# Performance work log

Hardware: AMD Instinct MI355X
Metric: run time of the kernel (lower is better)

## Reference

```python
import jax, jax.numpy as jnp
from jax import lax
import numpy as np

B, W, M, F = 8, 20, 512, 16
H = 128          # n_hidden
HALF = 64        # half_hid
K = 10           # conv out channels
LONG_K = W // 2  # dilated conv kernel


def setup_inputs() -> dict:
    key = jax.random.key(0)
    ks = jax.random.split(key, 24)
    s = 0.1  # weight scale (xavier-ish)
    return {
        "X": jax.random.normal(ks[0], (B, W, M, F), jnp.float32),
        "Y": jax.random.uniform(ks[1], (B, M), jnp.float32),
        "adj": jax.random.uniform(ks[2], (M, M), jnp.float32),
        "V": jax.random.normal(ks[3], (HALF,), jnp.float32) * s,
        "bv": jax.random.normal(ks[4], (1,), jnp.float32) * s,
        "W1": jax.random.normal(ks[5], (HALF, H), jnp.float32) * s,
        "b1": jax.random.normal(ks[6], (HALF,), jnp.float32) * s,
        "W2": jax.random.normal(ks[7], (HALF, H), jnp.float32) * s,
        "Wb": jax.random.normal(ks[8], (M, M), jnp.float32) * s,
        "wb": jax.random.normal(ks[9], (1,), jnp.float32) * s,
        "conv_w": jax.random.normal(ks[10], (K, F, W), jnp.float32) * s,
        "conv_b": jax.random.normal(ks[11], (K,), jnp.float32) * s,
        "convl_w": jax.random.normal(ks[12], (K, F, LONG_K), jnp.float32) * s,
        "convl_b": jax.random.normal(ks[13], (K,), jnp.float32) * s,
        "gru_Wih": jax.random.normal(ks[14], (3 * H, F), jnp.float32) * s,
        "gru_Whh": jax.random.normal(ks[15], (3 * H, H), jnp.float32) * s,
        "gru_bih": jax.random.normal(ks[16], (3 * H,), jnp.float32) * s,
        "gru_bhh": jax.random.normal(ks[17], (3 * H,), jnp.float32) * s,
        "gc1_W": jax.random.normal(ks[18], (3 * K, H), jnp.float32) * s,
        "gc1_b": jax.random.normal(ks[19], (H,), jnp.float32) * s,
        "gc2_W": jax.random.normal(ks[20], (H, K), jnp.float32) * s,
        "gc2_b": jax.random.normal(ks[21], (K,), jnp.float32) * s,
        "out_W": jax.random.normal(ks[22], (1, H + K), jnp.float32) * s,
        "out_b": jax.random.normal(ks[23], (1,), jnp.float32) * s,
    }


def _gru_last(xseq, Wih, Whh, bih, bhh):
    # xseq: (N, T, F) -> last hidden (N, H), PyTorch GRU gate order r,z,n
    n_hid = Whh.shape[1]
    def step(h, x_t):
        gx = x_t @ Wih.T + bih
        gh = h @ Whh.T + bhh
        xr, xz, xn = jnp.split(gx, 3, axis=-1)
        hr, hz, hn = jnp.split(gh, 3, axis=-1)
        r = jax.nn.sigmoid(xr + hr)
        z = jax.nn.sigmoid(xz + hz)
        n = jnp.tanh(xn + r * hn)
        return (1.0 - z) * n + z * h, None
    h0 = jnp.zeros((xseq.shape[0], n_hid), xseq.dtype)
    hT, _ = lax.scan(step, h0, jnp.moveaxis(xseq, 1, 0))
    return hT


def _forward(X, Y, adj, V, bv, W1, b1, W2, Wb, wb, conv_w, conv_b, convl_w,
             convl_b, gru_Wih, gru_Whh, gru_bih, gru_bhh, gc1_W, gc1_b,
             gc2_W, gc2_b, out_W, out_b):
    b, w, m, f = X.shape
    # ---- temporal branch: GRU per node ----
    x = jnp.transpose(X, (0, 2, 1, 3)).reshape(b * m, w, f)
    last_hid = _gru_last(x, gru_Wih, gru_Whh, gru_bih, gru_bhh).reshape(b, m, -1)
    out_temporal = last_hid
    # ---- attention-style adaptive adjacency ----
    # hid_rpt_m[b,i,j]=last_hid[b,j]; hid_rpt_w[b,i,j]=last_hid[b,i]
    p1 = jnp.einsum('bjh,kh->bjk', last_hid, W1)  # pairs with column index j
    p2 = jnp.einsum('bih,kh->bik', last_hid, W2)  # pairs with row index i
    pre = p1[:, None, :, :] + p2[:, :, None, :] + b1  # (b,m,m,half)
    a_mx = jnp.einsum('bijk,k->bij', jax.nn.elu(pre), V) + bv[0]
    # F.normalize(p=2, dim=1)
    nrm = jnp.sqrt(jnp.sum(a_mx * a_mx, axis=1, keepdims=True))
    a_mx = a_mx / jnp.maximum(nrm, 1e-12)
    # ---- per-node conv1d (vectorized over nodes) ----
    Xc = jnp.transpose(X, (0, 2, 3, 1)).reshape(b * m, f, w)  # (bm, f, w)
    dn = ('NCH', 'OIH', 'NCH')
    r = lax.conv_general_dilated(Xc, conv_w, (1,), 'VALID', dimension_numbers=dn)
    r = r + conv_b[None, :, None]                      # (bm, K, 1)
    rl = lax.conv_general_dilated(Xc, convl_w, (1,), 'VALID',
                                  rhs_dilation=(2,), dimension_numbers=dn)
    rl = rl + convl_b[None, :, None]                   # (bm, K, long_out)
    r_cat = jnp.concatenate([r, rl], axis=-1)          # (bm, K, 1+long_out)
    r_l = jax.nn.relu(r_cat.reshape(b, m, -1))         # (b, m, (1+long_out)*K)
    # ---- gate learned adjacency with fixed adjacency ----
    c = jax.nn.sigmoid(jnp.einsum('bij,jk->bik', a_mx, Wb) + wb[0])
    A = adj[None] * c + a_mx * (1.0 - c)               # (b,m,m)
    # ---- graph convolutions: out = A @ (x @ W) + b ----
    h1 = jax.nn.relu(jnp.einsum('bij,bjh->bih', A, r_l @ gc1_W) + gc1_b)
    out_spatial = jax.nn.relu(jnp.einsum('bij,bjh->bih', A, h1 @ gc2_W) + gc2_b)
    # ---- readout ----
    out = jnp.concatenate([out_spatial, out_temporal], axis=-1)
    out = (out @ out_W.T + out_b).squeeze(-1)          # (b, m)
    y = out.reshape(-1)
    Yf = Y.reshape(-1)
    # BCE with logits: softplus(y) - Y*y, averaged
    loss = jnp.mean(jax.nn.softplus(y) - Yf * y)
    return loss, jax.nn.sigmoid(y)


def reference(X, Y, adj, V, bv, W1, b1, W2, Wb, wb, conv_w, conv_b, convl_w,
              convl_b, gru_Wih, gru_Whh, gru_bih, gru_bhh, gc1_W, gc1_b,
              gc2_W, gc2_b, out_W, out_b):
    return _forward(X, Y, adj, V, bv, W1, b1, W2, Wb, wb, conv_w, conv_b,
                    convl_w, convl_b, gru_Wih, gru_Whh, gru_bih, gru_bhh,
                    gc1_W, gc1_b, gc2_W, gc2_b, out_W, out_b)
```

## Files before the change

kernel.cpp:

```cpp
#include <hip/hip_runtime.h>
#include <math.h>

#define Bn 8
#define Wn 20
#define Mn 512
#define Fn 16
#define Hn 128
#define HALFn 64
#define Kn 10

typedef __attribute__((ext_vector_type(8))) short short8;
typedef __attribute__((ext_vector_type(4))) float f32x4;
typedef unsigned short ushort_t;

__device__ __forceinline__ float sigmoidf_(float x) {
  return 1.0f / (1.0f + __expf(-x));
}
__device__ __forceinline__ float tanhf_(float x) {
  float xx = fminf(fmaxf(x, -15.f), 15.f);
  float e = __expf(2.f * xx);
  return (e - 1.f) / (e + 1.f);
}
__device__ __forceinline__ float reluf_(float x) { return fmaxf(x, 0.f); }
__device__ __forceinline__ float eluf_(float x) {
  return (x > 0.f) ? x : (__expf(x) - 1.f);
}
__device__ __forceinline__ ushort_t bf16_rne(float v) {
  unsigned u = __float_as_uint(v);
  u += 0x7FFFu + ((u >> 16) & 1u);
  return (ushort_t)(u >> 16);
}
__device__ __forceinline__ float bf16_to_f(ushort_t b) {
  return __uint_as_float(((unsigned)b) << 16);
}

__global__ __launch_bounds__(256) void pack_kernel(
    const float* __restrict__ Whh, const float* __restrict__ Wih,
    const float* __restrict__ Wb, ushort_t* __restrict__ Bpack,
    ushort_t* __restrict__ WbT_hi, ushort_t* __restrict__ WbT_lo,
    float* __restrict__ ssq, float* __restrict__ d_out) {
  int tid = threadIdx.x;
  if (blockIdx.x < 240) {
    int idx = blockIdx.x * 256 + tid;
    if (idx < 4096) ssq[idx] = 0.f;
    if (idx == 0) d_out[0] = 0.f;
    if (idx >= 24 * 5 * 512) return;
    int j = idx & 7;
    int lane = (idx >> 3) & 63;
    int ks = (idx >> 9) % 5;
    int nt = idx / (5 * 512);
    int k = ks * 32 + (lane >> 4) * 8 + j;
    int g = (nt & 7) * 16 + (nt >> 3) * 128 + (lane & 15);
    float val = 0.f;
    if (k < 128) val = Whh[g * 128 + k];
    else if (k < 144) val = Wih[g * 16 + (k - 128)];
    ushort_t hb = bf16_rne(val);
    float lo = val - bf16_to_f(hb);
    Bpack[(((long)nt * 5 + ks) * 2 + 0) * 512 + lane * 8 + j] = hb;
    Bpack[(((long)nt * 5 + ks) * 2 + 1) * 512 + lane * 8 + j] = bf16_rne(lo);
  } else {
    int t = blockIdx.x - 240;
    int k0 = (t >> 3) * 64, j0 = (t & 7) * 64;
    __shared__ float wt[64][65];
    for (int idx = tid; idx < 4096; idx += 256) {
      int r = idx >> 6, c = idx & 63;
      wt[r][c] = Wb[(long)(k0 + r) * 512 + j0 + c];
    }
    __syncthreads();
    for (int idx = tid; idx < 4096; idx += 256) {
      int r = idx >> 6, c = idx & 63;
      float v = wt[c][r];
      ushort_t hb = bf16_rne(v);
      WbT_hi[(long)(j0 + r) * 512 + k0 + c] = hb;
      WbT_lo[(long)(j0 + r) * 512 + k0 + c] = bf16_rne(v - bf16_to_f(hb));
    }
  }
}

#define LDK 168
#define HSZ (16 * LDK)
__global__ __launch_bounds__(512, 2) void gru_kernel(
    const float* __restrict__ X, const ushort_t* __restrict__ Bpack,
    const float* __restrict__ bih, const float* __restrict__ bhh,
    const float* __restrict__ W1, const float* __restrict__ W2,
    const float* __restrict__ b1, float* __restrict__ last_hid,
    float* __restrict__ p1, float* __restrict__ p2) {
  const int tid = threadIdx.x;
  const int wave = tid >> 6;
  const int lane = tid & 63;
  const int quad = lane >> 4;
  const int jl = lane & 15;
  const int j0 = wave * 16;
  const int blk = blockIdx.x;
  const int b = blk >> 5;
  const int m0 = (blk & 31) * 16;

  __shared__ __align__(16) ushort_t smem_hs[4 * HSZ];

  short8 frR[5][2], frZ[5][2], frN[4][2], frXN[2];
#pragma unroll
  for (int ks = 0; ks < 5; ++ks) {
#pragma unroll
    for (int p = 0; p < 2; ++p) {
      frR[ks][p] = *(const short8*)&Bpack[(((long)(wave) * 5 + ks) * 2 + p) * 512 + lane * 8];
      frZ[ks][p] = *(const short8*)&Bpack[(((long)(8 + wave) * 5 + ks) * 2 + p) * 512 + lane * 8];
    }
  }
#pragma unroll
  for (int ks = 0; ks < 4; ++ks) {
#pragma unroll
    for (int p = 0; p < 2; ++p)
      frN[ks][p] = *(const short8*)&Bpack[(((long)(16 + wave) * 5 + ks) * 2 + p) * 512 + lane * 8];
  }
#pragma unroll
  for (int p = 0; p < 2; ++p)
    frXN[p] = *(const short8*)&Bpack[(((long)(16 + wave) * 5 + 4) * 2 + p) * 512 + lane * 8];

  const float cr  = bih[j0 + jl] + bhh[j0 + jl];
  const float cz  = bih[128 + j0 + jl] + bhh[128 + j0 + jl];
  const float cnx = bih[256 + j0 + jl];
  const float cnh = bhh[256 + j0 + jl];

  for (int i = tid; i < 4 * HSZ; i += 512) smem_hs[i] = 0;

  const float* Xb = X + (long)b * (Wn * Mn * Fn) + (long)m0 * Fn;
  float x0 = 0.f;
  if (tid < 256) x0 = Xb[tid];
  __syncthreads();
  if (tid < 256) {
    int s = tid >> 4, f = tid & 15;
    ushort_t hb = bf16_rne(x0);
    smem_hs[0 * HSZ + s * LDK + 128 + f] = hb;
    smem_hs[2 * HSZ + s * LDK + 128 + f] = bf16_rne(x0 - bf16_to_f(hb));
  }
  __syncthreads();

  float hp[4] = {0.f, 0.f, 0.f, 0.f};

  for (int t = 0; t < Wn; ++t) {
    const int cur = t & 1, nxt = cur ^ 1;
    const int hiC = cur * HSZ, loC = (2 + cur) * HSZ;
    const int hiN = nxt * HSZ, loN = (2 + nxt) * HSZ;
    float xpre = 0.f;
    if (tid < 256 && t < Wn - 1) xpre = Xb[(long)(t + 1) * (Mn * Fn) + tid];

    f32x4 aR[2], aZ[2], aHN[2], aXN;
    aR[0] = aR[1] = aZ[0] = aZ[1] = aHN[0] = aHN[1] = aXN = (f32x4){0.f, 0.f, 0.f, 0.f};
#pragma unroll
    for (int ks = 0; ks < 5; ++ks) {
      const int p = ks & 1;
      short8 ah = *(const short8*)&smem_hs[hiC + jl * LDK + ks * 32 + quad * 8];
      short8 al = *(const short8*)&smem_hs[loC + jl * LDK + ks * 32 + quad * 8];
      aR[p] = __builtin_amdgcn_mfma_f32_16x16x32_bf16(ah, frR[ks][0], aR[p], 0, 0, 0);
      aR[p] = __builtin_amdgcn_mfma_f32_16x16x32_bf16(ah, frR[ks][1], aR[p], 0, 0, 0);
      aR[p] = __builtin_amdgcn_mfma_f32_16x16x32_bf16(al, frR[ks][0], aR[p], 0, 0, 0);
      aZ[p] = __builtin_amdgcn_mfma_f32_16x16x32_bf16(ah, frZ[ks][0], aZ[p], 0, 0, 0);
      aZ[p] = __builtin_amdgcn_mfma_f32_16x16x32_bf16(ah, frZ[ks][1], aZ[p], 0, 0, 0);
      aZ[p] = __builtin_amdgcn_mfma_f32_16x16x32_bf16(al, frZ[ks][0], aZ[p], 0, 0, 0);
      if (ks < 4) {
        aHN[p] = __builtin_amdgcn_mfma_f32_16x16x32_bf16(ah, frN[ks][0], aHN[p], 0, 0, 0);
        aHN[p] = __builtin_amdgcn_mfma_f32_16x16x32_bf16(ah, frN[ks][1], aHN[p], 0, 0, 0);
        aHN[p] = __builtin_amdgcn_mfma_f32_16x16x32_bf16(al, frN[ks][0], aHN[p], 0, 0, 0);
      } else {
        aXN = __builtin_amdgcn_mfma_f32_16x16x32_bf16(ah, frXN[0], aXN, 0, 0, 0);
        aXN = __builtin_amdgcn_mfma_f32_16x16x32_bf16(ah, frXN[1], aXN, 0, 0, 0);
        aXN = __builtin_amdgcn_mfma_f32_16x16x32_bf16(al, frXN[0], aXN, 0, 0, 0);
      }
    }

#pragma unroll
    for (int reg = 0; reg < 4; ++reg) {
      float r = sigmoidf_(aR[0][reg] + aR[1][reg] + cr);
      float z = sigmoidf_(aZ[0][reg] + aZ[1][reg] + cz);
      float n = tanhf_(aXN[reg] + cnx + r * (aHN[0][reg] + aHN[1][reg] + cnh));
      float h = (1.f - z) * n + z * hp[reg];
      hp[reg] = h;
      int s = quad * 4 + reg;
      ushort_t hb = bf16_rne(h);
      smem_hs[hiN + s * LDK + j0 + jl] = hb;
      smem_hs[loN + s * LDK + j0 + jl] = bf16_rne(h - bf16_to_f(hb));
    }
    if (tid < 256 && t < Wn - 1) {
      int s = tid >> 4, f = tid & 15;
      ushort_t hb = bf16_rne(xpre);
      smem_hs[hiN + s * LDK + 128 + f] = hb;
      smem_hs[loN + s * LDK + 128 + f] = bf16_rne(xpre - bf16_to_f(hb));
    }
    __syncthreads();
  }

  float* hs_f = (float*)smem_hs;
#pragma unroll
  for (int reg = 0; reg < 4; ++reg) {
    int s = quad * 4 + reg;
    float h = hp[reg];
    last_hid[(long)(blk * 16 + s) * Hn + j0 + jl] = h;
    hs_f[s * 132 + j0 + jl] = h;
  }
  __syncthreads();
  {
    int k = tid & 63;
    int part = (tid >> 6) & 1;
    int sg = tid >> 7;
    const float* Wp = part ? W2 : W1;
    float a[4];
    float init = part ? 0.f : b1[k];
    a[0] = a[1] = a[2] = a[3] = init;
    for (int h = 0; h < 128; h += 4) {
      float4 w = *(const float4*)&Wp[k * 128 + h];
#pragma unroll
      for (int rr = 0; rr < 4; ++rr) {
        float4 q = *(const float4*)&hs_f[(sg * 4 + rr) * 132 + h];
        a[rr] += q.x * w.x + q.y * w.y + q.z * w.z + q.w * w.w;
      }
    }
    float* outp = part ? p2 : p1;
#pragma unroll
    for (int rr = 0; rr < 4; ++rr)
      outp[(long)(blk * 16 + sg * 4 + rr) * 64 + k] = a[rr];
  }
}

__global__ __launch_bounds__(128) void conv_t1_kernel(
    const float* __restrict__ X, const float* __restrict__ conv_w,
    const float* __restrict__ conv_b, const float* __restrict__ convl_w,
    const float* __restrict__ convl_b, const float* __restrict__ gc1_W,
    ushort_t* __restrict__ t1T_hi, ushort_t* __restrict__ t1T_lo) {
  int tid = threadIdx.x;
  int n0 = blockIdx.x * 8;
  int b = n0 >> 9, m0 = n0 & 511;
  __shared__ float xs[8][16][20];
  __shared__ float cw[3200];
  __shared__ float clw[1600];
  __shared__ float rs[8][32];
  for (int idx = tid; idx < 3200; idx += 128) cw[idx] = conv_w[idx];
  for (int idx = tid; idx < 1600; idx += 128) clw[idx] = convl_w[idx];
  for (int w = 0; w < 20; ++w)
    xs[tid >> 4][tid & 15][w] = X[((long)(b * 20 + w) * 512 + m0) * 16 + tid];
  __syncthreads();
  if (tid < 80) {
    int s = tid / 10, k = tid % 10;
    float a0 = conv_b[k];
    float l0 = convl_b[k], l1 = convl_b[k];
    for (int f = 0; f < 16; ++f) {
#pragma unroll
      for (int w = 0; w < 20; ++w) a0 = fmaf(xs[s][f][w], cw[k * 320 + f * 20 + w], a0);
#pragma unroll
      for (int q = 0; q < 10; ++q) {
        float wv = clw[k * 160 + f * 10 + q];
        l0 = fmaf(xs[s][f][2 * q], wv, l0);
        l1 = fmaf(xs[s][f][2 * q + 1], wv, l1);
      }
    }
    rs[s][k * 3 + 0] = reluf_(a0);
    rs[s][k * 3 + 1] = reluf_(l0);
    rs[s][k * 3 + 2] = reluf_(l1);
  }
  __syncthreads();
  float w[30];
#pragma unroll
  for (int q = 0; q < 30; ++q) w[q] = gc1_W[q * 128 + tid];
  long base = ((long)b * 128 + tid) * 512 + m0;
#pragma unroll
  for (int s = 0; s < 8; ++s) {
    float a = 0.f;
#pragma unroll
    for (int q = 0; q < 30; ++q) a = fmaf(rs[s][q], w[q], a);
    ushort_t hb = bf16_rne(a);
    t1T_hi[base + s] = hb;
    t1T_lo[base + s] = bf16_rne(a - bf16_to_f(hb));
  }
}

__global__ __launch_bounds__(256) void amx_kernel(
    const float* __restrict__ p1, const float* __restrict__ p2,
    const float* __restrict__ V, const float* __restrict__ bv,
    float* __restrict__ amx, float* __restrict__ ssq) {
  int tid = threadIdx.x;
  int j0 = blockIdx.x * 32, i0 = blockIdx.y * 32, bz = blockIdx.z;
  __shared__ float p1s[32][68];
  __shared__ float p2s[32][68];
  __shared__ float Vs[64];
  __shared__ float cred[16][33];
  if (tid < 64) Vs[tid] = V[tid];
  {
    int rr = tid >> 3, c0 = (tid & 7) * 8;
    *(float4*)&p1s[rr][c0]     = *(const float4*)&p1[(long)(bz * 512 + j0 + rr) * 64 + c0];
    *(float4*)&p1s[rr][c0 + 4] = *(const float4*)&p1[(long)(bz * 512 + j0 + rr) * 64 + c0 + 4];
    *(float4*)&p2s[rr][c0]     = *(const float4*)&p2[(long)(bz * 512 + i0 + rr) * 64 + c0];
    *(float4*)&p2s[rr][c0 + 4] = *(const float4*)&p2[(long)(bz * 512 + i0 + rr) * 64 + c0 + 4];
  }
  __syncthreads();
  int r0 = tid >> 4, c0 = tid & 15;
  float acc[2][2] = {{0.f, 0.f}, {0.f, 0.f}};
  for (int k = 0; k < 64; ++k) {
    float vj0 = p1s[c0][k], vj1 = p1s[c0 + 16][k];
    float vi0 = p2s[r0][k], vi1 = p2s[r0 + 16][k];
    float vk = Vs[k];
    acc[0][0] = fmaf(eluf_(vj0 + vi0), vk, acc[0][0]);
    acc[0][1] = fmaf(eluf_(vj1 + vi0), vk, acc[0][1]);
    acc[1][0] = fmaf(eluf_(vj0 + vi1), vk, acc[1][0]);
    acc[1][1] = fmaf(eluf_(vj1 + vi1), vk, acc[1][1]);
  }
  float bvv = bv[0];
  float s2[2] = {0.f, 0.f};
#pragma unroll
  for (int a = 0; a < 2; ++a)
#pragma unroll
    for (int c = 0; c < 2; ++c) {
      float v = acc[a][c] + bvv;
      amx[((long)(bz * 512 + i0 + r0 + a * 16)) * 512 + j0 + c0 + c * 16] = v;
      s2[c] += v * v;
    }
  cred[r0][c0] = s2[0];
  cred[r0][c0 + 16] = s2[1];
  __syncthreads();
  if (tid < 32) {
    float s = 0.f;
#pragma unroll
    for (int p = 0; p < 16; ++p) s += cred[p][tid];
    atomicAdd(&ssq[bz * 512 + j0 + tid], s);
  }
}

#define CPK 40
__global__ __launch_bounds__(128, 2) void gemm_cA(
    const float* __restrict__ amx, const ushort_t* __restrict__ WbT_hi,
    const ushort_t* __restrict__ WbT_lo, const float* __restrict__ adj,
    const float* __restrict__ wb, const float* __restrict__ ssq,
    float* __restrict__ A) {
  const int bz = blockIdx.z;
  const int i0 = blockIdx.y * 128;
  const int j0 = blockIdx.x * 64;
  const int tid = threadIdx.x;
  const int wave = tid >> 6;
  const int lane = tid & 63;
  const int quad = lane >> 4, jl = lane & 15;

  __shared__ __align__(16) ushort_t Ahi[128][CPK];
  __shared__ __align__(16) ushort_t Alo[128][CPK];
  __shared__ __align__(16) ushort_t Bhi[64][CPK];
  __shared__ __align__(16) ushort_t Blo[64][CPK];
  __shared__ float rs_s[512];

  const float* Abase = amx + (long)bz * 262144;
  const float* sb = ssq + bz * 512;
  for (int i = tid; i < 512; i += 128)
    rs_s[i] = 1.f / fmaxf(sqrtf(sb[i]), 1e-12f);

  f32x4 acc[4][4];
#pragma unroll
  for (int a = 0; a < 4; ++a)
#pragma unroll
    for (int c = 0; c < 4; ++c) acc[a][c] = (f32x4){0.f, 0.f, 0.f, 0.f};

  for (int kk0 = 0; kk0 < 512; kk0 += 32) {
    __syncthreads();
#pragma unroll
    for (int l = 0; l < 8; ++l) {
      int e = l * 512 + tid * 4;
      int r = e >> 5, kq = e & 31;
      float4 v = *(const float4*)&Abase[(long)(i0 + r) * 512 + kk0 + kq];
      float4 sc = *(const float4*)&rs_s[kk0 + kq];
      float vv[4] = {v.x * sc.x, v.y * sc.y, v.z * sc.z, v.w * sc.w};
#pragma unroll
      for (int q = 0; q < 4; ++q) {
        ushort_t hb = bf16_rne(vv[q]);
        Ahi[r][kq + q] = hb;
        Alo[r][kq + q] = bf16_rne(vv[q] - bf16_to_f(hb));
      }
    }
#pragma unroll
    for (int l = 0; l < 2; ++l) {
      int e = l * 1024 + tid * 8;
      int r = e >> 5, kc = e & 31;
      *(uint4*)&Bhi[r][kc] = *(const uint4*)&WbT_hi[(long)(j0 + r) * 512 + kk0 + kc];
      *(uint4*)&Blo[r][kc] = *(const uint4*)&WbT_lo[(long)(j0 + r) * 512 + kk0 + kc];
    }
    __syncthreads();
    short8 ah[4], al[4], bh[4], bl[4];
#pragma unroll
    for (int tm = 0; tm < 4; ++tm) {
      ah[tm] = *(const short8*)&Ahi[wave * 64 + tm * 16 + jl][quad * 8];
      al[tm] = *(const short8*)&Alo[wave * 64 + tm * 16 + jl][quad * 8];
    }
#pragma unroll
    for (int tn = 0; tn < 4; ++tn) {
      bh[tn] = *(const short8*)&Bhi[tn * 16 + jl][quad * 8];
      bl[tn] = *(const short8*)&Blo[tn * 16 + jl][quad * 8];
    }
#pragma unroll
    for (int tm = 0; tm < 4; ++tm)
#pragma unroll
      for (int tn = 0; tn < 4; ++tn) {
        acc[tm][tn] = __builtin_amdgcn_mfma_f32_16x16x32_bf16(ah[tm], bh[tn], acc[tm][tn], 0, 0, 0);
        acc[tm][tn] = __builtin_amdgcn_mfma_f32_16x16x32_bf16(ah[tm], bl[tn], acc[tm][tn], 0, 0, 0);
        acc[tm][tn] = __builtin_amdgcn_mfma_f32_16x16x32_bf16(al[tm], bh[tn], acc[tm][tn], 0, 0, 0);
      }
  }

  const float wbv = wb[0];
#pragma unroll
  for (int tn = 0; tn < 4; ++tn) {
    int j = j0 + tn * 16 + jl;
    float sj = rs_s[j];
#pragma unroll
    for (int tm = 0; tm < 4; ++tm) {
#pragma unroll
      for (int reg = 0; reg < 4; ++reg) {
        int i = i0 + wave * 64 + tm * 16 + quad * 4 + reg;
        long ofs = (long)bz * 262144 + (long)i * 512 + j;
        float c = sigmoidf_(acc[tm][tn][reg] + wbv);
        float am = Abase[(long)i * 512 + j] * sj;
        float ad = adj[(long)i * 512 + j];
        A[ofs] = ad * c + am * (1.f - c);
      }
    }
  }
}

__global__ __launch_bounds__(256, 2) void gemm_h1t2(
    const float* __restrict__ A, const ushort_t* __restrict__ t1T_hi,
    const ushort_t* __restrict__ t1T_lo, const float* __restrict__ gc1_b,
    const float* __restrict__ gc2_W, float* __restrict__ t2) {
  const int bz = blockIdx.y;
  const int i0 = blockIdx.x * 16;
  const int tid = threadIdx.x;
  const int wave = tid >> 6;
  const int lane = tid & 63;
  const int quad = lane >> 4, jl = lane & 15;

  __shared__ __align__(16) ushort_t Ahi[16][CPK];
  __shared__ __align__(16) ushort_t Alo[16][CPK];
  __shared__ __align__(16) ushort_t Bhi[128][CPK];
  __shared__ __align__(16) ushort_t Blo[128][CPK];
  __shared__ float h1s[16][132];
  __shared__ float gw[1280];

  const float* Ab = A + (long)bz * 262144;
  for (int idx = tid; idx < 1280; idx += 256) gw[idx] = gc2_W[idx];

  f32x4 acc[2];
  acc[0] = acc[1] = (f32x4){0.f, 0.f, 0.f, 0.f};

  for (int kk0 = 0; kk0 < 512; kk0 += 32) {
    __syncthreads();
    {
      int e = tid * 2;
      int r = e >> 5, kq = e & 31;
      float2 v = *(const float2*)&Ab[(long)(i0 + r) * 512 + kk0 + kq];
      ushort_t hb0 = bf16_rne(v.x);
      Ahi[r][kq] = hb0;
      Alo[r][kq] = bf16_rne(v.x - bf16_to_f(hb0));
      ushort_t hb1 = bf16_rne(v.y);
      Ahi[r][kq + 1] = hb1;
      Alo[r][kq + 1] = bf16_rne(v.y - bf16_to_f(hb1));
    }
#pragma unroll
    for (int l = 0; l < 2; ++l) {
      int e = l * 2048 + tid * 8;
      int r = e >> 5, kc = e & 31;
      *(uint4*)&Bhi[r][kc] = *(const uint4*)&t1T_hi[((long)bz * 128 + r) * 512 + kk0 + kc];
      *(uint4*)&Blo[r][kc] = *(const uint4*)&t1T_lo[((long)bz * 128 + r) * 512 + kk0 + kc];
    }
    __syncthreads();
    short8 ah = *(const short8*)&Ahi[jl][quad * 8];
    short8 al = *(const short8*)&Alo[jl][quad * 8];
    short8 bh[2], bl[2];
#pragma unroll
    for (int tn = 0; tn < 2; ++tn) {
      bh[tn] = *(const short8*)&Bhi[wave * 32 + tn * 16 + jl][quad * 8];
      bl[tn] = *(const short8*)&Blo[wave * 32 + tn * 16 + jl][quad * 8];
    }
#pragma unroll
    for (int tn = 0; tn < 2; ++tn) {
      acc[tn] = __builtin_amdgcn_mfma_f32_16x16x32_bf16(ah, bh[tn], acc[tn], 0, 0, 0);
      acc[tn] = __builtin_amdgcn_mfma_f32_16x16x32_bf16(ah, bl[tn], acc[tn], 0, 0, 0);
      acc[tn] = __builtin_amdgcn_mfma_f32_16x16x32_bf16(al, bh[tn], acc[tn], 0, 0, 0);
    }
  }
  __syncthreads();
#pragma unroll
  for (int tn = 0; tn < 2; ++tn) {
    int n = wave * 32 + tn * 16 + jl;
    float bb = gc1_b[n];
#pragma unroll
    for (int reg = 0; reg < 4; ++reg) {
      int r = quad * 4 + reg;
      h1s[r][n] = reluf_(acc[tn][reg] + bb);
    }
  }
  __syncthreads();
  if (tid < 160) {
    int r = tid / 10, c = tid % 10;
    float a = 0.f;
#pragma unroll 4
    for (int k = 0; k < 128; ++k) a = fmaf(h1s[r][k], gw[k * 10 + c], a);
    t2[((long)bz * 512 + i0 + r) * 10 + c] = a;
  }
}

__global__ __launch_bounds__(256) void spat_readout(
    const float* __restrict__ A, const float* __restrict__ t2,
    const float* __restrict__ gc2_b, const float* __restrict__ last_hid,
    const float* __restrict__ out_W, const float* __restrict__ out_b,
    const float* __restrict__ Y, float* __restrict__ d_out) {
  int tid = threadIdx.x;
  int bz = blockIdx.y;
  int i0 = blockIdx.x * 16;
  __shared__ float t2s[5120];
  __shared__ float wS[138];
  __shared__ float osps[16][12];
  for (int idx = tid; idx < 5120; idx += 256) t2s[idx] = t2[(long)bz * 5120 + idx];
  for (int idx = tid; idx < 138; idx += 256) wS[idx] = out_W[idx];
  __syncthreads();
  int r = tid >> 4, sk = tid & 15;
  const float* Arow = A + (long)bz * 262144 + (long)(i0 + r) * 512;
  float acc[10] = {0, 0, 0, 0, 0, 0, 0, 0, 0, 0};
  for (int k = sk; k < 512; k += 16) {
    float av = Arow[k];
    const float* tp = &t2s[k * 10];
#pragma unroll
    for (int c = 0; c < 10; ++c) acc[c] = fmaf(av, tp[c], acc[c]);
  }
#pragma unroll
  for (int off = 8; off; off >>= 1)
#pragma unroll
    for (int c = 0; c < 10; ++c) acc[c] += __shfl_xor(acc[c], off);
  if (sk == 0) {
#pragma unroll
    for (int c = 0; c < 10; ++c) osps[r][c] = reluf_(acc[c] + gc2_b[c]);
  }
  __syncthreads();
  float l = 0.f;
  if (tid < 16) {
    int gid = bz * 512 + i0 + tid;
    float y = out_b[0];
#pragma unroll
    for (int k = 0; k < 10; ++k) y = fmaf(osps[tid][k], wS[k], y);
    const float* hp = &last_hid[(long)gid * 128];
    for (int h = 0; h < 128; h += 4) {
      float4 hv = *(const float4*)&hp[h];
      y = fmaf(hv.x, wS[10 + h + 0], y);
      y = fmaf(hv.y, wS[10 + h + 1], y);
      y = fmaf(hv.z, wS[10 + h + 2], y);
      y = fmaf(hv.w, wS[10 + h + 3], y);
    }
    d_out[1 + gid] = sigmoidf_(y);
    l = fmaxf(y, 0.f) + log1pf(__expf(-fabsf(y))) - Y[gid] * y;
  }
  if (tid < 64) {
#pragma unroll
    for (int off = 8; off; off >>= 1) l += __shfl_down(l, off);
    if (tid == 0) atomicAdd(d_out, l * (1.0f / 4096.f));
  }
}

extern "C" void kernel_launch(void* const* d_in, const int* in_sizes, int n_in,
                              void* d_out, int out_size, void* d_ws, size_t ws_size,
                              hipStream_t stream) {
  const float* X       = (const float*)d_in[0];
  const float* Y       = (const float*)d_in[1];
  const float* adj     = (const float*)d_in[2];
  const float* V       = (const float*)d_in[3];
  const float* bv      = (const float*)d_in[4];
  const float* W1      = (const float*)d_in[5];
  const float* b1      = (const float*)d_in[6];
  const float* W2      = (const float*)d_in[7];
  const float* Wb      = (const float*)d_in[8];
  const float* wb      = (const float*)d_in[9];
  const float* conv_w  = (const float*)d_in[10];
  const float* conv_b  = (const float*)d_in[11];
  const float* convl_w = (const float*)d_in[12];
  const float* convl_b = (const float*)d_in[13];
  const float* gWih    = (const float*)d_in[14];
  const float* gWhh    = (const float*)d_in[15];
  const float* gbih    = (const float*)d_in[16];
  const float* gbhh    = (const float*)d_in[17];
  const float* gc1_W   = (const float*)d_in[18];
  const float* gc1_b   = (const float*)d_in[19];
  const float* gc2_W   = (const float*)d_in[20];
  const float* gc2_b   = (const float*)d_in[21];
  const float* out_W   = (const float*)d_in[22];
  const float* out_b   = (const float*)d_in[23];
  float* out = (float*)d_out;

  float* ws = (float*)d_ws;
  float* lhid  = ws; ws += 524288;
  float* p1    = ws; ws += 262144;
  float* p2    = ws; ws += 262144;
  float* amx   = ws; ws += 2097152;
  float* ssq   = ws; ws += 4096;
  float* Abuf  = ws; ws += 2097152;
  float* t2    = ws; ws += 40960;
  float* Bpkf  = ws; ws += 122880;
  float* WbTf  = ws; ws += 262144;
  float* t1Tf  = ws; ws += 524288;
  if (ws_size < (size_t)(ws - (float*)d_ws) * sizeof(float)) return;
  ushort_t* Bpack  = (ushort_t*)Bpkf;
  ushort_t* WbT_hi = (ushort_t*)WbTf;
  ushort_t* WbT_lo = WbT_hi + 262144;
  ushort_t* t1T_hi = (ushort_t*)t1Tf;
  ushort_t* t1T_lo = t1T_hi + 524288;

  pack_kernel<<<304, 256, 0, stream>>>(gWhh, gWih, Wb, Bpack, WbT_hi, WbT_lo,
                                       ssq, out);
  gru_kernel<<<256, 512, 0, stream>>>(X, Bpack, gbih, gbhh, W1, W2, b1,
                                      lhid, p1, p2);
  conv_t1_kernel<<<512, 128, 0, stream>>>(X, conv_w, conv_b, convl_w, convl_b,
                                          gc1_W, t1T_hi, t1T_lo);
  amx_kernel<<<dim3(16, 16, 8), 256, 0, stream>>>(p1, p2, V, bv, amx, ssq);
  gemm_cA<<<dim3(8, 4, 8), 128, 0, stream>>>(amx, WbT_hi, WbT_lo, adj, wb,
                                             ssq, Abuf);
  gemm_h1t2<<<dim3(32, 8), 256, 0, stream>>>(Abuf, t1T_hi, t1T_lo, gc1_b,
                                             gc2_W, t2);
  spat_readout<<<dim3(32, 8), 256, 0, stream>>>(Abuf, t2, gc2_b, lhid,
                                                out_W, out_b, Y, out);
}
```

Measured before the change: 263.2 us.

## Fuse all stages into one cooperative persistent kernel with grid syncs

```diff
diff --git a/kernel.cpp b/kernel.cpp
--- a/kernel.cpp
+++ b/kernel.cpp
@@ -1,13 +1,14 @@
 #include <hip/hip_runtime.h>
+#include <hip/hip_cooperative_groups.h>
 #include <math.h>
+
+namespace cg = cooperative_groups;
 
 #define Bn 8
 #define Wn 20
 #define Mn 512
 #define Fn 16
 #define Hn 128
-#define HALFn 64
-#define Kn 10
 
 typedef __attribute__((ext_vector_type(8))) short short8;
 typedef __attribute__((ext_vector_type(4))) float f32x4;
@@ -34,586 +35,551 @@
   return __uint_as_float(((unsigned)b) << 16);
 }
 
-__global__ __launch_bounds__(256) void pack_kernel(
-    const float* __restrict__ Whh, const float* __restrict__ Wih,
-    const float* __restrict__ Wb, ushort_t* __restrict__ Bpack,
-    ushort_t* __restrict__ WbT_hi, ushort_t* __restrict__ WbT_lo,
-    float* __restrict__ ssq, float* __restrict__ d_out) {
-  int tid = threadIdx.x;
-  if (blockIdx.x < 240) {
-    int idx = blockIdx.x * 256 + tid;
-    if (idx < 4096) ssq[idx] = 0.f;
-    if (idx == 0) d_out[0] = 0.f;
-    if (idx >= 24 * 5 * 512) return;
-    int j = idx & 7;
-    int lane = (idx >> 3) & 63;
-    int ks = (idx >> 9) % 5;
-    int nt = idx / (5 * 512);
-    int k = ks * 32 + (lane >> 4) * 8 + j;
-    int g = (nt & 7) * 16 + (nt >> 3) * 128 + (lane & 15);
-    float val = 0.f;
-    if (k < 128) val = Whh[g * 128 + k];
-    else if (k < 144) val = Wih[g * 16 + (k - 128)];
-    ushort_t hb = bf16_rne(val);
-    float lo = val - bf16_to_f(hb);
-    Bpack[(((long)nt * 5 + ks) * 2 + 0) * 512 + lane * 8 + j] = hb;
-    Bpack[(((long)nt * 5 + ks) * 2 + 1) * 512 + lane * 8 + j] = bf16_rne(lo);
-  } else {
-    int t = blockIdx.x - 240;
-    int k0 = (t >> 3) * 64, j0 = (t & 7) * 64;
-    __shared__ float wt[64][65];
-    for (int idx = tid; idx < 4096; idx += 256) {
-      int r = idx >> 6, c = idx & 63;
-      wt[r][c] = Wb[(long)(k0 + r) * 512 + j0 + c];
-    }
-    __syncthreads();
-    for (int idx = tid; idx < 4096; idx += 256) {
-      int r = idx >> 6, c = idx & 63;
-      float v = wt[c][r];
-      ushort_t hb = bf16_rne(v);
-      WbT_hi[(long)(j0 + r) * 512 + k0 + c] = hb;
-      WbT_lo[(long)(j0 + r) * 512 + k0 + c] = bf16_rne(v - bf16_to_f(hb));
-    }
-  }
-}
+struct KArgs {
+  const float *X, *Y, *adj, *V, *bv, *W1, *b1, *W2, *Wb, *wb;
+  const float *conv_w, *conv_b, *convl_w, *convl_b;
+  const float *gWih, *gWhh, *gbih, *gbhh;
+  const float *gc1_W, *gc1_b, *gc2_W, *gc2_b, *out_W, *out_b;
+  const float *Y2;
+  float *out, *lhid, *p1, *p2, *amx, *ssq, *Abuf, *t2;
+  ushort_t *Bpack, *WbT_hi, *WbT_lo, *t1T_hi, *t1T_lo;
+};
 
 #define LDK 168
 #define HSZ (16 * LDK)
-__global__ __launch_bounds__(512, 2) void gru_kernel(
-    const float* __restrict__ X, const ushort_t* __restrict__ Bpack,
-    const float* __restrict__ bih, const float* __restrict__ bhh,
-    const float* __restrict__ W1, const float* __restrict__ W2,
-    const float* __restrict__ b1, float* __restrict__ last_hid,
-    float* __restrict__ p1, float* __restrict__ p2) {
+#define CPK 40
+#define SMEM_BYTES 41984
+
+__global__ __launch_bounds__(512, 2) void mega_kernel(KArgs a) {
+  cg::grid_group grid = cg::this_grid();
   const int tid = threadIdx.x;
+  const int blk = blockIdx.x;
   const int wave = tid >> 6;
   const int lane = tid & 63;
   const int quad = lane >> 4;
   const int jl = lane & 15;
-  const int j0 = wave * 16;
-  const int blk = blockIdx.x;
-  const int b = blk >> 5;
-  const int m0 = (blk & 31) * 16;
-
-  __shared__ __align__(16) ushort_t smem_hs[4 * HSZ];
-
-  short8 frR[5][2], frZ[5][2], frN[4][2], frXN[2];
-#pragma unroll
-  for (int ks = 0; ks < 5; ++ks) {
-#pragma unroll
-    for (int p = 0; p < 2; ++p) {
-      frR[ks][p] = *(const short8*)&Bpack[(((long)(wave) * 5 + ks) * 2 + p) * 512 + lane * 8];
-      frZ[ks][p] = *(const short8*)&Bpack[(((long)(8 + wave) * 5 + ks) * 2 + p) * 512 + lane * 8];
+  __shared__ __align__(16) char smem_u[SMEM_BYTES];
+
+  {
+    int gid = blk * 512 + tid;
+    if (gid < 4096) a.ssq[gid] = 0.f;
+    if (gid == 0) a.out[0] = 0.f;
+    if (gid < 24 * 5 * 512) {
+      int j = gid & 7;
+      int ln = (gid >> 3) & 63;
+      int ks = (gid >> 9) % 5;
+      int nt = gid / (5 * 512);
+      int k = ks * 32 + (ln >> 4) * 8 + j;
+      int g = (nt & 7) * 16 + (nt >> 3) * 128 + (ln & 15);
+      float val = 0.f;
+      if (k < 128) val = a.gWhh[g * 128 + k];
+      else if (k < 144) val = a.gWih[g * 16 + (k - 128)];
+      ushort_t hb = bf16_rne(val);
+      a.Bpack[(((long)nt * 5 + ks) * 2 + 0) * 512 + ln * 8 + j] = hb;
+      a.Bpack[(((long)nt * 5 + ks) * 2 + 1) * 512 + ln * 8 + j] =
+          bf16_rne(val - bf16_to_f(hb));
+    }
+    float* xs  = (float*)smem_u;
+    float* cw  = (float*)(smem_u + 20480);
+    float* clw = (float*)(smem_u + 33280);
+    float* rs  = (float*)(smem_u + 39680);
+    int n0 = blk * 16;
+    int b = n0 >> 9, m0 = n0 & 511;
+    for (int idx = tid; idx < 3200; idx += 512) cw[idx] = a.conv_w[idx];
+    for (int idx = tid; idx < 1600; idx += 512) clw[idx] = a.convl_w[idx];
+    if (tid < 256) {
+      int s = tid >> 4, f = tid & 15;
+      for (int w = 0; w < 20; ++w)
+        xs[(s * 16 + f) * 20 + w] = a.X[((long)(b * 20 + w) * 512 + m0) * 16 + tid];
+    }
+    __syncthreads();
+    if (tid < 160) {
+      int s = tid / 10, k = tid % 10;
+      float a0 = a.conv_b[k];
+      float l0 = a.convl_b[k], l1 = a.convl_b[k];
+      for (int f = 0; f < 16; ++f) {
+#pragma unroll
+        for (int w = 0; w < 20; ++w)
+          a0 = fmaf(xs[(s * 16 + f) * 20 + w], cw[k * 320 + f * 20 + w], a0);
+#pragma unroll
+        for (int q = 0; q < 10; ++q) {
+          float wv = clw[k * 160 + f * 10 + q];
+          l0 = fmaf(xs[(s * 16 + f) * 20 + 2 * q], wv, l0);
+          l1 = fmaf(xs[(s * 16 + f) * 20 + 2 * q + 1], wv, l1);
+        }
+      }
+      rs[s * 32 + k * 3 + 0] = reluf_(a0);
+      rs[s * 32 + k * 3 + 1] = reluf_(l0);
+      rs[s * 32 + k * 3 + 2] = reluf_(l1);
+    }
+    __syncthreads();
+    {
+      int col = tid & 127, grp = tid >> 7;
+      float w[30];
+#pragma unroll
+      for (int q = 0; q < 30; ++q) w[q] = a.gc1_W[q * 128 + col];
+      long base = ((long)b * 128 + col) * 512 + m0;
+#pragma unroll
+      for (int ss = 0; ss < 4; ++ss) {
+        int s = grp * 4 + ss;
+        float acc = 0.f;
+#pragma unroll
+        for (int q = 0; q < 30; ++q) acc = fmaf(rs[s * 32 + q], w[q], acc);
+        ushort_t hb = bf16_rne(acc);
+        a.t1T_hi[base + s] = hb;
+        a.t1T_lo[base + s] = bf16_rne(acc - bf16_to_f(hb));
+      }
+    }
+    if (blk < 64) {
+      __syncthreads();
+      float* wt = (float*)smem_u;
+      int k0 = (blk >> 3) * 64, j0w = (blk & 7) * 64;
+      for (int idx = tid; idx < 4096; idx += 512) {
+        int r = idx >> 6, c = idx & 63;
+        wt[r * 65 + c] = a.Wb[(long)(k0 + r) * 512 + j0w + c];
+      }
+      __syncthreads();
+      for (int idx = tid; idx < 4096; idx += 512) {
+        int r = idx >> 6, c = idx & 63;
+        float v = wt[c * 65 + r];
+        ushort_t hb = bf16_rne(v);
+        a.WbT_hi[(long)(j0w + r) * 512 + k0 + c] = hb;
+        a.WbT_lo[(long)(j0w + r) * 512 + k0 + c] = bf16_rne(v - bf16_to_f(hb));
+      }
     }
   }
-#pragma unroll
-  for (int ks = 0; ks < 4; ++ks) {
+  __threadfence();
+  grid.sync();
+
+  {
+    ushort_t* smem_hs = (ushort_t*)smem_u;
+    const int j0 = wave * 16;
+    const int b = blk >> 5;
+    const int m0 = (blk & 31) * 16;
+
+    short8 frR[5][2], frZ[5][2], frN[4][2], frXN[2];
+#pragma unroll
+    for (int ks = 0; ks < 5; ++ks)
+#pragma unroll
+      for (int p = 0; p < 2; ++p) {
+        frR[ks][p] = *(const short8*)&a.Bpack[(((long)(wave) * 5 + ks) * 2 + p) * 512 + lane * 8];
+        frZ[ks][p] = *(const short8*)&a.Bpack[(((long)(8 + wave) * 5 + ks) * 2 + p) * 512 + lane * 8];
+      }
+#pragma unroll
+    for (int ks = 0; ks < 4; ++ks)
+#pragma unroll
+      for (int p = 0; p < 2; ++p)
+        frN[ks][p] = *(const short8*)&a.Bpack[(((long)(16 + wave) * 5 + ks) * 2 + p) * 512 + lane * 8];
 #pragma unroll
     for (int p = 0; p < 2; ++p)
-      frN[ks][p] = *(const short8*)&Bpack[(((long)(16 + wave) * 5 + ks) * 2 + p) * 512 + lane * 8];
+      frXN[p] = *(const short8*)&a.Bpack[(((long)(16 + wave) * 5 + 4) * 2 + p) * 512 + lane * 8];
+
+    const float cr  = a.gbih[j0 + jl] + a.gbhh[j0 + jl];
+    const float cz  = a.gbih[128 + j0 + jl] + a.gbhh[128 + j0 + jl];
+    const float cnx = a.gbih[256 + j0 + jl];
+    const float cnh = a.gbhh[256 + j0 + jl];
+
+    for (int i = tid; i < 4 * HSZ; i += 512) smem_hs[i] = 0;
+
+    const float* Xb = a.X + (long)b * (Wn * Mn * Fn) + (long)m0 * Fn;
+    float x0 = 0.f;
+    if (tid < 256) x0 = Xb[tid];
+    __syncthreads();
+    if (tid < 256) {
+      int s = tid >> 4, f = tid & 15;
+      ushort_t hb = bf16_rne(x0);
+      smem_hs[0 * HSZ + s * LDK + 128 + f] = hb;
+      smem_hs[2 * HSZ + s * LDK + 128 + f] = bf16_rne(x0 - bf16_to_f(hb));
+    }
+    __syncthreads();
+
+    float hp[4] = {0.f, 0.f, 0.f, 0.f};
+    for (int t = 0; t < Wn; ++t) {
+      const int cur = t & 1, nxt = cur ^ 1;
+      const int hiC = cur * HSZ, loC = (2 + cur) * HSZ;
+      const int hiN = nxt * HSZ, loN = (2 + nxt) * HSZ;
+      float xpre = 0.f;
+      if (tid < 256 && t < Wn - 1) xpre = Xb[(long)(t + 1) * (Mn * Fn) + tid];
+
+      f32x4 aR[2], aZ[2], aHN[2], aXN;
+      aR[0] = aR[1] = aZ[0] = aZ[1] = aHN[0] = aHN[1] = aXN = (f32x4){0.f, 0.f, 0.f, 0.f};
+#pragma unroll
+      for (int ks = 0; ks < 5; ++ks) {
+        const int p = ks & 1;
+        short8 ah = *(const short8*)&smem_hs[hiC + jl * LDK + ks * 32 + quad * 8];
+        short8 al = *(const short8*)&smem_hs[loC + jl * LDK + ks * 32 + quad * 8];
+        aR[p] = __builtin_amdgcn_mfma_f32_16x16x32_bf16(ah, frR[ks][0], aR[p], 0, 0, 0);
+        aR[p] = __builtin_amdgcn_mfma_f32_16x16x32_bf16(ah, frR[ks][1], aR[p], 0, 0, 0);
+        aR[p] = __builtin_amdgcn_mfma_f32_16x16x32_bf16(al, frR[ks][0], aR[p], 0, 0, 0);
+        aZ[p] = __builtin_amdgcn_mfma_f32_16x16x32_bf16(ah, frZ[ks][0], aZ[p], 0, 0, 0);
+        aZ[p] = __builtin_amdgcn_mfma_f32_16x16x32_bf16(ah, frZ[ks][1], aZ[p], 0, 0, 0);
+        aZ[p] = __builtin_amdgcn_mfma_f32_16x16x32_bf16(al, frZ[ks][0], aZ[p], 0, 0, 0);
+        if (ks < 4) {
+          aHN[p] = __builtin_amdgcn_mfma_f32_16x16x32_bf16(ah, frN[ks][0], aHN[p], 0, 0, 0);
+          aHN[p] = __builtin_amdgcn_mfma_f32_16x16x32_bf16(ah, frN[ks][1], aHN[p], 0, 0, 0);
+          aHN[p] = __builtin_amdgcn_mfma_f32_16x16x32_bf16(al, frN[ks][0], aHN[p], 0, 0, 0);
+        } else {
+          aXN = __builtin_amdgcn_mfma_f32_16x16x32_bf16(ah, frXN[0], aXN, 0, 0, 0);
+          aXN = __builtin_amdgcn_mfma_f32_16x16x32_bf16(ah, frXN[1], aXN, 0, 0, 0);
+          aXN = __builtin_amdgcn_mfma_f32_16x16x32_bf16(al, frXN[0], aXN, 0, 0, 0);
+        }
+      }
+#pragma unroll
+      for (int reg = 0; reg < 4; ++reg) {
+        float r = sigmoidf_(aR[0][reg] + aR[1][reg] + cr);
+        float z = sigmoidf_(aZ[0][reg] + aZ[1][reg] + cz);
+        float n = tanhf_(aXN[reg] + cnx + r * (aHN[0][reg] + aHN[1][reg] + cnh));
+        float h = (1.f - z) * n + z * hp[reg];
+        hp[reg] = h;
+        int s = quad * 4 + reg;
+        ushort_t hb = bf16_rne(h);
+        smem_hs[hiN + s * LDK + j0 + jl] = hb;
+        smem_hs[loN + s * LDK + j0 + jl] = bf16_rne(h - bf16_to_f(hb));
+      }
+      if (tid < 256 && t < Wn - 1) {
+        int s = tid >> 4, f = tid & 15;
+        ushort_t hb = bf16_rne(xpre);
+        smem_hs[hiN + s * LDK + 128 + f] = hb;
+        smem_hs[loN + s * LDK + 128 + f] = bf16_rne(xpre - bf16_to_f(hb));
+      }
+      __syncthreads();
+    }
+
+    float* hs_f = (float*)smem_u;
+#pragma unroll
+    for (int reg = 0; reg < 4; ++reg) {
+      int s = quad * 4 + reg;
+      float h = hp[reg];
+      a.lhid[(long)(blk * 16 + s) * Hn + j0 + jl] = h;
+      hs_f[s * 132 + j0 + jl] = h;
+    }
+    __syncthreads();
+    {
+      int k = tid & 63;
+      int part = (tid >> 6) & 1;
+      int sg = tid >> 7;
+      const float* Wp = part ? a.W2 : a.W1;
+      float acc[4];
+      float init = part ? 0.f : a.b1[k];
+      acc[0] = acc[1] = acc[2] = acc[3] = init;
+      for (int h = 0; h < 128; h += 4) {
+        float4 w = *(const float4*)&Wp[k * 128 + h];
+#pragma unroll
+        for (int rr = 0; rr < 4; ++rr) {
+          float4 q = *(const float4*)&hs_f[(sg * 4 + rr) * 132 + h];
+          acc[rr] += q.x * w.x + q.y * w.y + q.z * w.z + q.w * w.w;
+        }
+      }
+      float* outp = part ? a.p2 : a.p1;
+#pragma unroll
+      for (int rr = 0; rr < 4; ++rr)
+        outp[(long)(blk * 16 + sg * 4 + rr) * 64 + k] = acc[rr];
+    }
   }
-#pragma unroll
-  for (int p = 0; p < 2; ++p)
-    frXN[p] = *(const short8*)&Bpack[(((long)(16 + wave) * 5 + 4) * 2 + p) * 512 + lane * 8];
-
-  const float cr  = bih[j0 + jl] + bhh[j0 + jl];
-  const float cz  = bih[128 + j0 + jl] + bhh[128 + j0 + jl];
-  const float cnx = bih[256 + j0 + jl];
-  const float cnh = bhh[256 + j0 + jl];
-
-  for (int i = tid; i < 4 * HSZ; i += 512) smem_hs[i] = 0;
-
-  const float* Xb = X + (long)b * (Wn * Mn * Fn) + (long)m0 * Fn;
-  float x0 = 0.f;
-  if (tid < 256) x0 = Xb[tid];
-  __syncthreads();
-  if (tid < 256) {
-    int s = tid >> 4, f = tid & 15;
-    ushort_t hb = bf16_rne(x0);
-    smem_hs[0 * HSZ + s * LDK + 128 + f] = hb;
-    smem_hs[2 * HSZ + s * LDK + 128 + f] = bf16_rne(x0 - bf16_to_f(hb));
+  __threadfence();
+  grid.sync();
+
+  {
+    float* Vs   = (float*)smem_u;
+    float* p1s  = (float*)(smem_u + 256);
+    float* p2s  = (float*)(smem_u + 256 + 17408);
+    float* cred = (float*)(smem_u + 256 + 34816);
+    int half = tid >> 8, t = tid & 255;
+    if (tid < 64) Vs[tid] = a.V[tid];
+    float* P1 = p1s + half * 2176;
+    float* P2 = p2s + half * 2176;
+    float* CR = cred + half * 528;
+    for (int pass = 0; pass < 4; ++pass) {
+      int tile = blk * 8 + pass * 2 + half;
+      int bz = tile >> 8, by = (tile >> 4) & 15, bx = tile & 15;
+      int i0 = by * 32, j0 = bx * 32;
+      __syncthreads();
+      {
+        int rr = t >> 3, c0 = (t & 7) * 8;
+        *(float4*)&P1[rr * 68 + c0]     = *(const float4*)&a.p1[(long)(bz * 512 + j0 + rr) * 64 + c0];
+        *(float4*)&P1[rr * 68 + c0 + 4] = *(const float4*)&a.p1[(long)(bz * 512 + j0 + rr) * 64 + c0 + 4];
+        *(float4*)&P2[rr * 68 + c0]     = *(const float4*)&a.p2[(long)(bz * 512 + i0 + rr) * 64 + c0];
+        *(float4*)&P2[rr * 68 + c0 + 4] = *(const float4*)&a.p2[(long)(bz * 512 + i0 + rr) * 64 + c0 + 4];
+      }
+      __syncthreads();
+      int r0 = t >> 4, c0 = t & 15;
+      float acc[2][2] = {{0.f, 0.f}, {0.f, 0.f}};
+      for (int k = 0; k < 64; ++k) {
+        float vj0 = P1[c0 * 68 + k], vj1 = P1[(c0 + 16) * 68 + k];
+        float vi0 = P2[r0 * 68 + k], vi1 = P2[(r0 + 16) * 68 + k];
+        float vk = Vs[k];
+        acc[0][0] = fmaf(eluf_(vj0 + vi0), vk, acc[0][0]);
+        acc[0][1] = fmaf(eluf_(vj1 + vi0), vk, acc[0][1]);
+        acc[1][0] = fmaf(eluf_(vj0 + vi1), vk, acc[1][0]);
+        acc[1][1] = fmaf(eluf_(vj1 + vi1), vk, acc[1][1]);
+      }
+      float bvv = a.bv[0];
+      float s2[2] = {0.f, 0.f};
+#pragma unroll
+      for (int aa = 0; aa < 2; ++aa)
+#pragma unroll
+        for (int c = 0; c < 2; ++c) {
+          float v = acc[aa][c] + bvv;
+          a.amx[((long)(bz * 512 + i0 + r0 + aa * 16)) * 512 + j0 + c0 + c * 16] = v;
+          s2[c] += v * v;
+        }
+      CR[r0 * 33 + c0] = s2[0];
+      CR[r0 * 33 + c0 + 16] = s2[1];
+      __syncthreads();
+      if (t < 32) {
+        float s = 0.f;
+#pragma unroll
+        for (int p = 0; p < 16; ++p) s += CR[p * 33 + t];
+        atomicAdd(&a.ssq[bz * 512 + j0 + t], s);
+      }
+    }
   }
-  __syncthreads();
-
-  float hp[4] = {0.f, 0.f, 0.f, 0.f};
-
-  for (int t = 0; t < Wn; ++t) {
-    const int cur = t & 1, nxt = cur ^ 1;
-    const int hiC = cur * HSZ, loC = (2 + cur) * HSZ;
-    const int hiN = nxt * HSZ, loN = (2 + nxt) * HSZ;
-    float xpre = 0.f;
-    if (tid < 256 && t < Wn - 1) xpre = Xb[(long)(t + 1) * (Mn * Fn) + tid];
-
-    f32x4 aR[2], aZ[2], aHN[2], aXN;
-    aR[0] = aR[1] = aZ[0] = aZ[1] = aHN[0] = aHN[1] = aXN = (f32x4){0.f, 0.f, 0.f, 0.f};
-#pragma unroll
-    for (int ks = 0; ks < 5; ++ks) {
-      const int p = ks & 1;
-      short8 ah = *(const short8*)&smem_hs[hiC + jl * LDK + ks * 32 + quad * 8];
-      short8 al = *(const short8*)&smem_hs[loC + jl * LDK + ks * 32 + quad * 8];
-      aR[p] = __builtin_amdgcn_mfma_f32_16x16x32_bf16(ah, frR[ks][0], aR[p], 0, 0, 0);
-      aR[p] = __builtin_amdgcn_mfma_f32_16x16x32_bf16(ah, frR[ks][1], aR[p], 0, 0, 0);
-      aR[p] = __builtin_amdgcn_mfma_f32_16x16x32_bf16(al, frR[ks][0], aR[p], 0, 0, 0);
-      aZ[p] = __builtin_amdgcn_mfma_f32_16x16x32_bf16(ah, frZ[ks][0], aZ[p], 0, 0, 0);
-      aZ[p] = __builtin_amdgcn_mfma_f32_16x16x32_bf16(ah, frZ[ks][1], aZ[p], 0, 0, 0);
-      aZ[p] = __builtin_amdgcn_mfma_f32_16x16x32_bf16(al, frZ[ks][0], aZ[p], 0, 0, 0);
-      if (ks < 4) {
-        aHN[p] = __builtin_amdgcn_mfma_f32_16x16x32_bf16(ah, frN[ks][0], aHN[p], 0, 0, 0);
-        aHN[p] = __builtin_amdgcn_mfma_f32_16x16x32_bf16(ah, frN[ks][1], aHN[p], 0, 0, 0);
-        aHN[p] = __builtin_amdgcn_mfma_f32_16x16x32_bf16(al, frN[ks][0], aHN[p], 0, 0, 0);
-      } else {
-        aXN = __builtin_amdgcn_mfma_f32_16x16x32_bf16(ah, frXN[0], aXN, 0, 0, 0);
-        aXN = __builtin_amdgcn_mfma_f32_16x16x32_bf16(ah, frXN[1], aXN, 0, 0, 0);
-        aXN = __builtin_amdgcn_mfma_f32_16x16x32_bf16(al, frXN[0], aXN, 0, 0, 0);
-      }
-    }
-
-#pragma unroll
-    for (int reg = 0; reg < 4; ++reg) {
-      float r = sigmoidf_(aR[0][reg] + aR[1][reg] + cr);
-      float z = sigmoidf_(aZ[0][reg] + aZ[1][reg] + cz);
-      float n = tanhf_(aXN[reg] + cnx + r * (aHN[0][reg] + aHN[1][reg] + cnh));
-      float h = (1.f - z) * n + z * hp[reg];
-      hp[reg] = h;
-      int s = quad * 4 + reg;
-      ushort_t hb = bf16_rne(h);
-      smem_hs[hiN + s * LDK + j0 + jl] = hb;
-      smem_hs[loN + s * LDK + j0 + jl] = bf16_rne(h - bf16_to_f(hb));
-    }
-    if (tid < 256 && t < Wn - 1) {
-      int s = tid >> 4, f = tid & 15;
-      ushort_t hb = bf16_rne(xpre);
-      smem_hs[hiN + s * LDK + 128 + f] = hb;
-      smem_hs[loN + s * LDK + 128 + f] = bf16_rne(xpre - bf16_to_f(hb));
-    }
-    __syncthreads();
+  __threadfence();
+  grid.sync();
+
+  {
+    ushort_t* Ahi = (ushort_t*)smem_u;
+    ushort_t* Alo = (ushort_t*)(smem_u + 10240);
+    ushort_t* Bhi = (ushort_t*)(smem_u + 20480);
+    ushort_t* Blo = (ushort_t*)(smem_u + 25600);
+    float*    rsS = (float*)(smem_u + 30720);
+    int bx = blk & 7, by = (blk >> 3) & 3, bz = blk >> 5;
+    int i0 = by * 128, j0 = bx * 64;
+    const float* Abase = a.amx + (long)bz * 262144;
+    const float* sb = a.ssq + bz * 512;
+    rsS[tid] = 1.f / fmaxf(sqrtf(sb[tid]), 1e-12f);
+
+    f32x4 acc[4];
+#pragma unroll
+    for (int c = 0; c < 4; ++c) acc[c] = (f32x4){0.f, 0.f, 0.f, 0.f};
+
+    for (int kk0 = 0; kk0 < 512; kk0 += 32) {
+      __syncthreads();
+#pragma unroll
+      for (int l = 0; l < 2; ++l) {
+        int e = l * 2048 + tid * 4;
+        int r = e >> 5, kq = e & 31;
+        float4 v = *(const float4*)&Abase[(long)(i0 + r) * 512 + kk0 + kq];
+        float4 sc = *(const float4*)&rsS[kk0 + kq];
+        float vv[4] = {v.x * sc.x, v.y * sc.y, v.z * sc.z, v.w * sc.w};
+#pragma unroll
+        for (int q = 0; q < 4; ++q) {
+          ushort_t hb = bf16_rne(vv[q]);
+          Ahi[r * CPK + kq + q] = hb;
+          Alo[r * CPK + kq + q] = bf16_rne(vv[q] - bf16_to_f(hb));
+        }
+      }
+      if (tid < 256) {
+        int e = tid * 8;
+        int r = e >> 5, kc = e & 31;
+        *(uint4*)&Bhi[r * CPK + kc] = *(const uint4*)&a.WbT_hi[(long)(j0 + r) * 512 + kk0 + kc];
+        *(uint4*)&Blo[r * CPK + kc] = *(const uint4*)&a.WbT_lo[(long)(j0 + r) * 512 + kk0 + kc];
+      }
+      __syncthreads();
+      short8 ah = *(const short8*)&Ahi[(wave * 16 + jl) * CPK + quad * 8];
+      short8 al = *(const short8*)&Alo[(wave * 16 + jl) * CPK + quad * 8];
+      short8 bh[4], bl[4];
+#pragma unroll
+      for (int tn = 0; tn < 4; ++tn) {
+        bh[tn] = *(const short8*)&Bhi[(tn * 16 + jl) * CPK + quad * 8];
+        bl[tn] = *(const short8*)&Blo[(tn * 16 + jl) * CPK + quad * 8];
+      }
+#pragma unroll
+      for (int tn = 0; tn < 4; ++tn) {
+        acc[tn] = __builtin_amdgcn_mfma_f32_16x16x32_bf16(ah, bh[tn], acc[tn], 0, 0, 0);
+        acc[tn] = __builtin_amdgcn_mfma_f32_16x16x32_bf16(ah, bl[tn], acc[tn], 0, 0, 0);
+        acc[tn] = __builtin_amdgcn_mfma_f32_16x16x32_bf16(al, bh[tn], acc[tn], 0, 0, 0);
+      }
+    }
+    const float wbv = a.wb[0];
+#pragma unroll
+    for (int tn = 0; tn < 4; ++tn) {
+      int j = j0 + tn * 16 + jl;
+      float sj = rsS[j];
+#pragma unroll
+      for (int reg = 0; reg < 4; ++reg) {
+        int i = i0 + wave * 16 + quad * 4 + reg;
+        long ofs = (long)bz * 262144 + (long)i * 512 + j;
+        float c = sigmoidf_(acc[tn][reg] + wbv);
+        float am = Abase[(long)i * 512 + j] * sj;
+        float ad = a.adj[(long)i * 512 + j];
+        a.Abuf[ofs] = ad * c + am * (1.f - c);
+      }
+    }
   }
-
-  float* hs_f = (float*)smem_hs;
-#pragma unroll
-  for (int reg = 0; reg < 4; ++reg) {
-    int s = quad * 4 + reg;
-    float h = hp[reg];
-    last_hid[(long)(blk * 16 + s) * Hn + j0 + jl] = h;
-    hs_f[s * 132 + j0 + jl] = h;
+  __threadfence();
+  grid.sync();
+
+  {
+    ushort_t* Ahi = (ushort_t*)smem_u;
+    ushort_t* Alo = (ushort_t*)(smem_u + 1280);
+    ushort_t* Bhi = (ushort_t*)(smem_u + 2560);
+    ushort_t* Blo = (ushort_t*)(smem_u + 12800);
+    float*    h1s = (float*)(smem_u + 23040);
+    float*    gw  = (float*)(smem_u + 31488);
+    int ib = blk & 31, bz = blk >> 5;
+    int i0 = ib * 16;
+    const float* Ab = a.Abuf + (long)bz * 262144;
+    for (int idx = tid; idx < 1280; idx += 512) gw[idx] = a.gc2_W[idx];
+
+    f32x4 acc[2];
+    acc[0] = acc[1] = (f32x4){0.f, 0.f, 0.f, 0.f};
+    for (int kk0 = 0; kk0 < 512; kk0 += 32) {
+      __syncthreads();
+      {
+        int r = tid >> 5, kq = tid & 31;
+        float v = Ab[(long)(i0 + r) * 512 + kk0 + kq];
+        ushort_t hb = bf16_rne(v);
+        Ahi[r * CPK + kq] = hb;
+        Alo[r * CPK + kq] = bf16_rne(v - bf16_to_f(hb));
+      }
+      {
+        int e = tid * 8;
+        int r = e >> 5, kc = e & 31;
+        *(uint4*)&Bhi[r * CPK + kc] = *(const uint4*)&a.t1T_hi[((long)bz * 128 + r) * 512 + kk0 + kc];
+        *(uint4*)&Blo[r * CPK + kc] = *(const uint4*)&a.t1T_lo[((long)bz * 128 + r) * 512 + kk0 + kc];
+      }
+      __syncthreads();
+      if (wave < 4) {
+        short8 ah = *(const short8*)&Ahi[jl * CPK + quad * 8];
+        short8 al = *(const short8*)&Alo[jl * CPK + quad * 8];
+#pragma unroll
+        for (int tn = 0; tn < 2; ++tn) {
+          short8 bh = *(const short8*)&Bhi[(wave * 32 + tn * 16 + jl) * CPK + quad * 8];
+          short8 bl = *(const short8*)&Blo[(wave * 32 + tn * 16 + jl) * CPK + quad * 8];
+          acc[tn] = __builtin_amdgcn_mfma_f32_16x16x32_bf16(ah, bh, acc[tn], 0, 0, 0);
+          acc[tn] = __builtin_amdgcn_mfma_f32_16x16x32_bf16(ah, bl, acc[tn], 0, 0, 0);
+          acc[tn] = __builtin_amdgcn_mfma_f32_16x16x32_bf16(al, bh, acc[tn], 0, 0, 0);
+        }
+      }
+    }
+    __syncthreads();
+    if (wave < 4) {
+#pragma unroll
+      for (int tn = 0; tn < 2; ++tn) {
+        int n = wave * 32 + tn * 16 + jl;
+        float bb = a.gc1_b[n];
+#pragma unroll
+        for (int reg = 0; reg < 4; ++reg) {
+          int r = quad * 4 + reg;
+          h1s[r * 132 + n] = reluf_(acc[tn][reg] + bb);
+        }
+      }
+    }
+    __syncthreads();
+    if (tid < 160) {
+      int r = tid / 10, c = tid % 10;
+      float s = 0.f;
+#pragma unroll 4
+      for (int k = 0; k < 128; ++k) s = fmaf(h1s[r * 132 + k], gw[k * 10 + c], s);
+      a.t2[((long)bz * 512 + i0 + r) * 10 + c] = s;
+    }
   }
-  __syncthreads();
+  __threadfence();
+  grid.sync();
+
   {
-    int k = tid & 63;
-    int part = (tid >> 6) & 1;
-    int sg = tid >> 7;
-    const float* Wp = part ? W2 : W1;
-    float a[4];
-    float init = part ? 0.f : b1[k];
-    a[0] = a[1] = a[2] = a[3] = init;
-    for (int h = 0; h < 128; h += 4) {
-      float4 w = *(const float4*)&Wp[k * 128 + h];
-#pragma unroll
-      for (int rr = 0; rr < 4; ++rr) {
-        float4 q = *(const float4*)&hs_f[(sg * 4 + rr) * 132 + h];
-        a[rr] += q.x * w.x + q.y * w.y + q.z * w.z + q.w * w.w;
-      }
-    }
-    float* outp = part ? p2 : p1;
-#pragma unroll
-    for (int rr = 0; rr < 4; ++rr)
-      outp[(long)(blk * 16 + sg * 4 + rr) * 64 + k] = a[rr];
-  }
-}
-
-__global__ __launch_bounds__(128) void conv_t1_kernel(
-    const float* __restrict__ X, const float* __restrict__ conv_w,
-    const float* __restrict__ conv_b, const float* __restrict__ convl_w,
-    const float* __restrict__ convl_b, const float* __restrict__ gc1_W,
-    ushort_t* __restrict__ t1T_hi, ushort_t* __restrict__ t1T_lo) {
-  int tid = threadIdx.x;
-  int n0 = blockIdx.x * 8;
-  int b = n0 >> 9, m0 = n0 & 511;
-  __shared__ float xs[8][16][20];
-  __shared__ float cw[3200];
-  __shared__ float clw[1600];
-  __shared__ float rs[8][32];
-  for (int idx = tid; idx < 3200; idx += 128) cw[idx] = conv_w[idx];
-  for (int idx = tid; idx < 1600; idx += 128) clw[idx] = convl_w[idx];
-  for (int w = 0; w < 20; ++w)
-    xs[tid >> 4][tid & 15][w] = X[((long)(b * 20 + w) * 512 + m0) * 16 + tid];
-  __syncthreads();
-  if (tid < 80) {
-    int s = tid / 10, k = tid % 10;
-    float a0 = conv_b[k];
-    float l0 = convl_b[k], l1 = convl_b[k];
-    for (int f = 0; f < 16; ++f) {
-#pragma unroll
-      for (int w = 0; w < 20; ++w) a0 = fmaf(xs[s][f][w], cw[k * 320 + f * 20 + w], a0);
-#pragma unroll
-      for (int q = 0; q < 10; ++q) {
-        float wv = clw[k * 160 + f * 10 + q];
-        l0 = fmaf(xs[s][f][2 * q], wv, l0);
-        l1 = fmaf(xs[s][f][2 * q + 1], wv, l1);
-      }
-    }
-    rs[s][k * 3 + 0] = reluf_(a0);
-    rs[s][k * 3 + 1] = reluf_(l0);
-    rs[s][k * 3 + 2] = reluf_(l1);
-  }
-  __syncthreads();
-  float w[30];
-#pragma unroll
-  for (int q = 0; q < 30; ++q) w[q] = gc1_W[q * 128 + tid];
-  long base = ((long)b * 128 + tid) * 512 + m0;
-#pragma unroll
-  for (int s = 0; s < 8; ++s) {
-    float a = 0.f;
-#pragma unroll
-    for (int q = 0; q < 30; ++q) a = fmaf(rs[s][q], w[q], a);
-    ushort_t hb = bf16_rne(a);
-    t1T_hi[base + s] = hb;
-    t1T_lo[base + s] = bf16_rne(a - bf16_to_f(hb));
-  }
-}
-
-__global__ __launch_bounds__(256) void amx_kernel(
-    const float* __restrict__ p1, const float* __restrict__ p2,
-    const float* __restrict__ V, const float* __restrict__ bv,
-    float* __restrict__ amx, float* __restrict__ ssq) {
-  int tid = threadIdx.x;
-  int j0 = blockIdx.x * 32, i0 = blockIdx.y * 32, bz = blockIdx.z;
-  __shared__ float p1s[32][68];
-  __shared__ float p2s[32][68];
-  __shared__ float Vs[64];
-  __shared__ float cred[16][33];
-  if (tid < 64) Vs[tid] = V[tid];
-  {
-    int rr = tid >> 3, c0 = (tid & 7) * 8;
-    *(float4*)&p1s[rr][c0]     = *(const float4*)&p1[(long)(bz * 512 + j0 + rr) * 64 + c0];
-    *(float4*)&p1s[rr][c0 + 4] = *(const float4*)&p1[(long)(bz * 512 + j0 + rr) * 64 + c0 + 4];
-    *(float4*)&p2s[rr][c0]     = *(const float4*)&p2[(long)(bz * 512 + i0 + rr) * 64 + c0];
-    *(float4*)&p2s[rr][c0 + 4] = *(const float4*)&p2[(long)(bz * 512 + i0 + rr) * 64 + c0 + 4];
-  }
-  __syncthreads();
-  int r0 = tid >> 4, c0 = tid & 15;
-  float acc[2][2] = {{0.f, 0.f}, {0.f, 0.f}};
-  for (int k = 0; k < 64; ++k) {
-    float vj0 = p1s[c0][k], vj1 = p1s[c0 + 16][k];
-    float vi0 = p2s[r0][k], vi1 = p2s[r0 + 16][k];
-    float vk = Vs[k];
-    acc[0][0] = fmaf(eluf_(vj0 + vi0), vk, acc[0][0]);
-    acc[0][1] = fmaf(eluf_(vj1 + vi0), vk, acc[0][1]);
-    acc[1][0] = fmaf(eluf_(vj0 + vi1), vk, acc[1][0]);
-    acc[1][1] = fmaf(eluf_(vj1 + vi1), vk, acc[1][1]);
-  }
-  float bvv = bv[0];
-  float s2[2] = {0.f, 0.f};
-#pragma unroll
-  for (int a = 0; a < 2; ++a)
-#pragma unroll
-    for (int c = 0; c < 2; ++c) {
-      float v = acc[a][c] + bvv;
-      amx[((long)(bz * 512 + i0 + r0 + a * 16)) * 512 + j0 + c0 + c * 16] = v;
-      s2[c] += v * v;
-    }
-  cred[r0][c0] = s2[0];
-  cred[r0][c0 + 16] = s2[1];
-  __syncthreads();
-  if (tid < 32) {
-    float s = 0.f;
-#pragma unroll
-    for (int p = 0; p < 16; ++p) s += cred[p][tid];
-    atomicAdd(&ssq[bz * 512 + j0 + tid], s);
-  }
-}
-
-#define CPK 40
-__global__ __launch_bounds__(128, 2) void gemm_cA(
-    const float* __restrict__ amx, const ushort_t* __restrict__ WbT_hi,
-    const ushort_t* __restrict__ WbT_lo, const float* __restrict__ adj,
-    const float* __restrict__ wb, const float* __restrict__ ssq,
-    float* __restrict__ A) {
-  const int bz = blockIdx.z;
-  const int i0 = blockIdx.y * 128;
-  const int j0 = blockIdx.x * 64;
-  const int tid = threadIdx.x;
-  const int wave = tid >> 6;
-  const int lane = tid & 63;
-  const int quad = lane >> 4, jl = lane & 15;
-
-  __shared__ __align__(16) ushort_t Ahi[128][CPK];
-  __shared__ __align__(16) ushort_t Alo[128][CPK];
-  __shared__ __align__(16) ushort_t Bhi[64][CPK];
-  __shared__ __align__(16) ushort_t Blo[64][CPK];
-  __shared__ float rs_s[512];
-
-  const float* Abase = amx + (long)bz * 262144;
-  const float* sb = ssq + bz * 512;
-  for (int i = tid; i < 512; i += 128)
-    rs_s[i] = 1.f / fmaxf(sqrtf(sb[i]), 1e-12f);
-
-  f32x4 acc[4][4];
-#pragma unroll
-  for (int a = 0; a < 4; ++a)
-#pragma unroll
-    for (int c = 0; c < 4; ++c) acc[a][c] = (f32x4){0.f, 0.f, 0.f, 0.f};
-
-  for (int kk0 = 0; kk0 < 512; kk0 += 32) {
-    __syncthreads();
-#pragma unroll
-    for (int l = 0; l < 8; ++l) {
-      int e = l * 512 + tid * 4;
-      int r = e >> 5, kq = e & 31;
-      float4 v = *(const float4*)&Abase[(long)(i0 + r) * 512 + kk0 + kq];
-      float4 sc = *(const float4*)&rs_s[kk0 + kq];
-      float vv[4] = {v.x * sc.x, v.y * sc.y, v.z * sc.z, v.w * sc.w};
-#pragma unroll
-      for (int q = 0; q < 4; ++q) {
-        ushort_t hb = bf16_rne(vv[q]);
-        Ahi[r][kq + q] = hb;
-        Alo[r][kq + q] = bf16_rne(vv[q] - bf16_to_f(hb));
-      }
-    }
-#pragma unroll
-    for (int l = 0; l < 2; ++l) {
-      int e = l * 1024 + tid * 8;
-      int r = e >> 5, kc = e & 31;
-      *(uint4*)&Bhi[r][kc] = *(const uint4*)&WbT_hi[(long)(j0 + r) * 512 + kk0 + kc];
-      *(uint4*)&Blo[r][kc] = *(const uint4*)&WbT_lo[(long)(j0 + r) * 512 + kk0 + kc];
-    }
-    __syncthreads();
-    short8 ah[4], al[4], bh[4], bl[4];
-#pragma unroll
-    for (int tm = 0; tm < 4; ++tm) {
-      ah[tm] = *(const short8*)&Ahi[wave * 64 + tm * 16 + jl][quad * 8];
-      al[tm] = *(const short8*)&Alo[wave * 64 + tm * 16 + jl][quad * 8];
-    }
-#pragma unroll
-    for (int tn = 0; tn < 4; ++tn) {
-      bh[tn] = *(const short8*)&Bhi[tn * 16 + jl][quad * 8];
-      bl[tn] = *(const short8*)&Blo[tn * 16 + jl][quad * 8];
-    }
-#pragma unroll
-    for (int tm = 0; tm < 4; ++tm)
-#pragma unroll
-      for (int tn = 0; tn < 4; ++tn) {
-        acc[tm][tn] = __builtin_amdgcn_mfma_f32_16x16x32_bf16(ah[tm], bh[tn], acc[tm][tn], 0, 0, 0);
-        acc[tm][tn] = __builtin_amdgcn_mfma_f32_16x16x32_bf16(ah[tm], bl[tn], acc[tm][tn], 0, 0, 0);
-        acc[tm][tn] = __builtin_amdgcn_mfma_f32_16x16x32_bf16(al[tm], bh[tn], acc[tm][tn], 0, 0, 0);
-      }
-  }
-
-  const float wbv = wb[0];
-#pragma unroll
-  for (int tn = 0; tn < 4; ++tn) {
-    int j = j0 + tn * 16 + jl;
-    float sj = rs_s[j];
-#pragma unroll
-    for (int tm = 0; tm < 4; ++tm) {
-#pragma unroll
-      for (int reg = 0; reg < 4; ++reg) {
-        int i = i0 + wave * 64 + tm * 16 + quad * 4 + reg;
-        long ofs = (long)bz * 262144 + (long)i * 512 + j;
-        float c = sigmoidf_(acc[tm][tn][reg] + wbv);
-        float am = Abase[(long)i * 512 + j] * sj;
-        float ad = adj[(long)i * 512 + j];
-        A[ofs] = ad * c + am * (1.f - c);
-      }
-    }
-  }
-}
-
-__global__ __launch_bounds__(256, 2) void gemm_h1t2(
-    const float* __restrict__ A, const ushort_t* __restrict__ t1T_hi,
-    const ushort_t* __restrict__ t1T_lo, const float* __restrict__ gc1_b,
-    const float* __restrict__ gc2_W, float* __restrict__ t2) {
-  const int bz = blockIdx.y;
-  const int i0 = blockIdx.x * 16;
-  const int tid = threadIdx.x;
-  const int wave = tid >> 6;
-  const int lane = tid & 63;
-  const int quad = lane >> 4, jl = lane & 15;
-
-  __shared__ __align__(16) ushort_t Ahi[16][CPK];
-  __shared__ __align__(16) ushort_t Alo[16][CPK];
-  __shared__ __align__(16) ushort_t Bhi[128][CPK];
-  __shared__ __align__(16) ushort_t Blo[128][CPK];
-  __shared__ float h1s[16][132];
-  __shared__ float gw[1280];
-
-  const float* Ab = A + (long)bz * 262144;
-  for (int idx = tid; idx < 1280; idx += 256) gw[idx] = gc2_W[idx];
-
-  f32x4 acc[2];
-  acc[0] = acc[1] = (f32x4){0.f, 0.f, 0.f, 0.f};
-
-  for (int kk0 = 0; kk0 < 512; kk0 += 32) {
-    __syncthreads();
-    {
-      int e = tid * 2;
-      int r = e >> 5, kq = e & 31;
-      float2 v = *(const float2*)&Ab[(long)(i0 + r) * 512 + kk0 + kq];
-      ushort_t hb0 = bf16_rne(v.x);
-      Ahi[r][kq] = hb0;
-      Alo[r][kq] = bf16_rne(v.x - bf16_to_f(hb0));
-      ushort_t hb1 = bf16_rne(v.y);
-      Ahi[r][kq + 1] = hb1;
-      Alo[r][kq + 1] = bf16_rne(v.y - bf16_to_f(hb1));
-    }
-#pragma unroll
-    for (int l = 0; l < 2; ++l) {
-      int e = l * 2048 + tid * 8;
-      int r = e >> 5, kc = e & 31;
-      *(uint4*)&Bhi[r][kc] = *(const uint4*)&t1T_hi[((long)bz * 128 + r) * 512 + kk0 + kc];
-      *(uint4*)&Blo[r][kc] = *(const uint4*)&t1T_lo[((long)bz * 128 + r) * 512 + kk0 + kc];
-    }
-    __syncthreads();
-    short8 ah = *(const short8*)&Ahi[jl][quad * 8];
-    short8 al = *(const short8*)&Alo[jl][quad * 8];
-    short8 bh[2], bl[2];
-#pragma unroll
-    for (int tn = 0; tn < 2; ++tn) {
-      bh[tn] = *(const short8*)&Bhi[wave * 32 + tn * 16 + jl][quad * 8];
-      bl[tn] = *(const short8*)&Blo[wave * 32 + tn * 16 + jl][quad * 8];
-    }
-#pragma unroll
-    for (int tn = 0; tn < 2; ++tn) {
-      acc[tn] = __builtin_amdgcn_mfma_f32_16x16x32_bf16(ah, bh[tn], acc[tn], 0, 0, 0);
-      acc[tn] = __builtin_amdgcn_mfma_f32_16x16x32_bf16(ah, bl[tn], acc[tn], 0, 0, 0);
-      acc[tn] = __builtin_amdgcn_mfma_f32_16x16x32_bf16(al, bh[tn], acc[tn], 0, 0, 0);
-    }
-  }
-  __syncthreads();
-#pragma unroll
-  for (int tn = 0; tn < 2; ++tn) {
-    int n = wave * 32 + tn * 16 + jl;
-    float bb = gc1_b[n];
-#pragma unroll
-    for (int reg = 0; reg < 4; ++reg) {
-      int r = quad * 4 + reg;
-      h1s[r][n] = reluf_(acc[tn][reg] + bb);
-    }
-  }
-  __syncthreads();
-  if (tid < 160) {
-    int r = tid / 10, c = tid % 10;
-    float a = 0.f;
-#pragma unroll 4
-    for (int k = 0; k < 128; ++k) a = fmaf(h1s[r][k], gw[k * 10 + c], a);
-    t2[((long)bz * 512 + i0 + r) * 10 + c] = a;
-  }
-}
-
-__global__ __launch_bounds__(256) void spat_readout(
-    const float* __restrict__ A, const float* __restrict__ t2,
-    const float* __restrict__ gc2_b, const float* __restrict__ last_hid,
-    const float* __restrict__ out_W, const float* __restrict__ out_b,
-    const float* __restrict__ Y, float* __restrict__ d_out) {
-  int tid = threadIdx.x;
-  int bz = blockIdx.y;
-  int i0 = blockIdx.x * 16;
-  __shared__ float t2s[5120];
-  __shared__ float wS[138];
-  __shared__ float osps[16][12];
-  for (int idx = tid; idx < 5120; idx += 256) t2s[idx] = t2[(long)bz * 5120 + idx];
-  for (int idx = tid; idx < 138; idx += 256) wS[idx] = out_W[idx];
-  __syncthreads();
-  int r = tid >> 4, sk = tid & 15;
-  const float* Arow = A + (long)bz * 262144 + (long)(i0 + r) * 512;
-  float acc[10] = {0, 0, 0, 0, 0, 0, 0, 0, 0, 0};
-  for (int k = sk; k < 512; k += 16) {
-    float av = Arow[k];
-    const float* tp = &t2s[k * 10];
-#pragma unroll
-    for (int c = 0; c < 10; ++c) acc[c] = fmaf(av, tp[c], acc[c]);
-  }
-#pragma unroll
-  for (int off = 8; off; off >>= 1)
-#pragma unroll
-    for (int c = 0; c < 10; ++c) acc[c] += __shfl_xor(acc[c], off);
-  if (sk == 0) {
-#pragma unroll
-    for (int c = 0; c < 10; ++c) osps[r][c] = reluf_(acc[c] + gc2_b[c]);
-  }
-  __syncthreads();
-  float l = 0.f;
-  if (tid < 16) {
-    int gid = bz * 512 + i0 + tid;
-    float y = out_b[0];
-#pragma unroll
-    for (int k = 0; k < 10; ++k) y = fmaf(osps[tid][k], wS[k], y);
-    const float* hp = &last_hid[(long)gid * 128];
-    for (int h = 0; h < 128; h += 4) {
-      float4 hv = *(const float4*)&hp[h];
-      y = fmaf(hv.x, wS[10 + h + 0], y);
-      y = fmaf(hv.y, wS[10 + h + 1], y);
-      y = fmaf(hv.z, wS[10 + h + 2], y);
-      y = fmaf(hv.w, wS[10 + h + 3], y);
-    }
-    d_out[1 + gid] = sigmoidf_(y);
-    l = fmaxf(y, 0.f) + log1pf(__expf(-fabsf(y))) - Y[gid] * y;
-  }
-  if (tid < 64) {
-#pragma unroll
-    for (int off = 8; off; off >>= 1) l += __shfl_down(l, off);
-    if (tid == 0) atomicAdd(d_out, l * (1.0f / 4096.f));
+    float* t2s  = (float*)smem_u;
+    float* wS   = (float*)(smem_u + 20480);
+    float* osps = (float*)(smem_u + 21056);
+    int ib = blk & 31, bz = blk >> 5;
+    int i0 = ib * 16;
+    for (int idx = tid; idx < 5120; idx += 512) t2s[idx] = a.t2[(long)bz * 5120 + idx];
+    for (int idx = tid; idx < 138; idx += 512) wS[idx] = a.out_W[idx];
+    __syncthreads();
+    int r = tid >> 5, sk = tid & 31;
+    const float* Arow = a.Abuf + (long)bz * 262144 + (long)(i0 + r) * 512;
+    float acc[10] = {0, 0, 0, 0, 0, 0, 0, 0, 0, 0};
+    for (int k = sk; k < 512; k += 32) {
+      float av = Arow[k];
+      const float* tp = &t2s[k * 10];
+#pragma unroll
+      for (int c = 0; c < 10; ++c) acc[c] = fmaf(av, tp[c], acc[c]);
+    }
+#pragma unroll
+    for (int off = 16; off; off >>= 1)
+#pragma unroll
+      for (int c = 0; c < 10; ++c) acc[c] += __shfl_xor(acc[c], off);
+    if (sk == 0) {
+#pragma unroll
+      for (int c = 0; c < 10; ++c) osps[r * 12 + c] = reluf_(acc[c] + a.gc2_b[c]);
+    }
+    __syncthreads();
+    float l = 0.f;
+    if (tid < 16) {
+      int gid = bz * 512 + i0 + tid;
+      float y = a.out_b[0];
+#pragma unroll
+      for (int k = 0; k < 10; ++k) y = fmaf(osps[tid * 12 + k], wS[k], y);
+      const float* hp = &a.lhid[(long)gid * 128];
+      for (int h = 0; h < 128; h += 4) {
+        float4 hv = *(const float4*)&hp[h];
+        y = fmaf(hv.x, wS[10 + h + 0], y);
+        y = fmaf(hv.y, wS[10 + h + 1], y);
+        y = fmaf(hv.z, wS[10 + h + 2], y);
+        y = fmaf(hv.w, wS[10 + h + 3], y);
+      }
+      a.out[1 + gid] = sigmoidf_(y);
+      l = fmaxf(y, 0.f) + log1pf(__expf(-fabsf(y))) - a.Y[gid] * y;
+    }
+    if (tid < 64) {
+#pragma unroll
+      for (int off = 8; off; off >>= 1) l += __shfl_down(l, off);
+      if (tid == 0) atomicAdd(a.out, l * (1.0f / 4096.f));
+    }
   }
 }
 
 extern "C" void kernel_launch(void* const* d_in, const int* in_sizes, int n_in,
                               void* d_out, int out_size, void* d_ws, size_t ws_size,
                               hipStream_t stream) {
-  const float* X       = (const float*)d_in[0];
-  const float* Y       = (const float*)d_in[1];
-  const float* adj     = (const float*)d_in[2];
-  const float* V       = (const float*)d_in[3];
-  const float* bv      = (const float*)d_in[4];
-  const float* W1      = (const float*)d_in[5];
-  const float* b1      = (const float*)d_in[6];
-  const float* W2      = (const float*)d_in[7];
-  const float* Wb      = (const float*)d_in[8];
-  const float* wb      = (const float*)d_in[9];
-  const float* conv_w  = (const float*)d_in[10];
-  const float* conv_b  = (const float*)d_in[11];
-  const float* convl_w = (const float*)d_in[12];
-  const float* convl_b = (const float*)d_in[13];
-  const float* gWih    = (const float*)d_in[14];
-  const float* gWhh    = (const float*)d_in[15];
-  const float* gbih    = (const float*)d_in[16];
-  const float* gbhh    = (const float*)d_in[17];
-  const float* gc1_W   = (const float*)d_in[18];
-  const float* gc1_b   = (const float*)d_in[19];
-  const float* gc2_W   = (const float*)d_in[20];
-  const float* gc2_b   = (const float*)d_in[21];
-  const float* out_W   = (const float*)d_in[22];
-  const float* out_b   = (const float*)d_in[23];
-  float* out = (float*)d_out;
+  KArgs ka;
+  ka.X       = (const float*)d_in[0];
+  ka.Y       = (const float*)d_in[1];
+  ka.adj     = (const float*)d_in[2];
+  ka.V       = (const float*)d_in[3];
+  ka.bv      = (const float*)d_in[4];
+  ka.W1      = (const float*)d_in[5];
+  ka.b1      = (const float*)d_in[6];
+  ka.W2      = (const float*)d_in[7];
+  ka.Wb      = (const float*)d_in[8];
+  ka.wb      = (const float*)d_in[9];
+  ka.conv_w  = (const float*)d_in[10];
+  ka.conv_b  = (const float*)d_in[11];
+  ka.convl_w = (const float*)d_in[12];
+  ka.convl_b = (const float*)d_in[13];
+  ka.gWih    = (const float*)d_in[14];
+  ka.gWhh    = (const float*)d_in[15];
+  ka.gbih    = (const float*)d_in[16];
+  ka.gbhh    = (const float*)d_in[17];
+  ka.gc1_W   = (const float*)d_in[18];
+  ka.gc1_b   = (const float*)d_in[19];
+  ka.gc2_W   = (const float*)d_in[20];
+  ka.gc2_b   = (const float*)d_in[21];
+  ka.out_W   = (const float*)d_in[22];
+  ka.out_b   = (const float*)d_in[23];
+  ka.Y2      = (const float*)d_in[1];
+  ka.out = (float*)d_out;
 
   float* ws = (float*)d_ws;
-  float* lhid  = ws; ws += 524288;
-  float* p1    = ws; ws += 262144;
-  float* p2    = ws; ws += 262144;
-  float* amx   = ws; ws += 2097152;
-  float* ssq   = ws; ws += 4096;
-  float* Abuf  = ws; ws += 2097152;
-  float* t2    = ws; ws += 40960;
-  float* Bpkf  = ws; ws += 122880;
-  float* WbTf  = ws; ws += 262144;
-  float* t1Tf  = ws; ws += 524288;
+  ka.lhid = ws; ws += 524288;
+  ka.p1   = ws; ws += 262144;
+  ka.p2   = ws; ws += 262144;
+  ka.amx  = ws; ws += 2097152;
+  ka.ssq  = ws; ws += 4096;
+  ka.Abuf = ws; ws += 2097152;
+  ka.t2   = ws; ws += 40960;
+  float* Bpkf = ws; ws += 122880;
+  float* WbTf = ws; ws += 262144;
+  float* t1Tf = ws; ws += 524288;
   if (ws_size < (size_t)(ws - (float*)d_ws) * sizeof(float)) return;
-  ushort_t* Bpack  = (ushort_t*)Bpkf;
-  ushort_t* WbT_hi = (ushort_t*)WbTf;
-  ushort_t* WbT_lo = WbT_hi + 262144;
-  ushort_t* t1T_hi = (ushort_t*)t1Tf;
-  ushort_t* t1T_lo = t1T_hi + 524288;
-
-  pack_kernel<<<304, 256, 0, stream>>>(gWhh, gWih, Wb, Bpack, WbT_hi, WbT_lo,
-                                       ssq, out);
-  gru_kernel<<<256, 512, 0, stream>>>(X, Bpack, gbih, gbhh, W1, W2, b1,
-                                      lhid, p1, p2);
-  conv_t1_kernel<<<512, 128, 0, stream>>>(X, conv_w, conv_b, convl_w, convl_b,
-                                          gc1_W, t1T_hi, t1T_lo);
-  amx_kernel<<<dim3(16, 16, 8), 256, 0, stream>>>(p1, p2, V, bv, amx, ssq);
-  gemm_cA<<<dim3(8, 4, 8), 128, 0, stream>>>(amx, WbT_hi, WbT_lo, adj, wb,
-                                             ssq, Abuf);
-  gemm_h1t2<<<dim3(32, 8), 256, 0, stream>>>(Abuf, t1T_hi, t1T_lo, gc1_b,
-                                             gc2_W, t2);
-  spat_readout<<<dim3(32, 8), 256, 0, stream>>>(Abuf, t2, gc2_b, lhid,
-                                                out_W, out_b, Y, out);
-}
+  ka.Bpack  = (ushort_t*)Bpkf;
+  ka.WbT_hi = (ushort_t*)WbTf;
+  ka.WbT_lo = ka.WbT_hi + 262144;
+  ka.t1T_hi = (ushort_t*)t1Tf;
+  ka.t1T_lo = ka.t1T_hi + 524288;
+
+  void* kargs[] = {(void*)&ka};
+  hipLaunchCooperativeKernel((const void*)mega_kernel, dim3(256), dim3(512),
+                             kargs, 0, stream);
+}
```

Measured after the change: 658.8 us. 150% more time.
